# Kernel tuning notes

Measured on AMD Instinct MI355X. Metric: run time of the kernel, lower is better.

Reference implementation:

```python
import jax, jax.numpy as jnp
import numpy as np
import math

NUM_HEADS = 16
SEGMENT_SIZE = 128
DILATION = 2


def hilbert_map(seq_len: int) -> np.ndarray:
    """Boustrophedon ('Hilbert') permutation, matching the torch reference."""
    if seq_len <= 64:
        return np.arange(seq_len, dtype=np.int64)
    g = int(math.ceil(math.sqrt(seq_len)))
    fm = np.zeros(seq_len, dtype=np.int64)
    idx = 0
    for row in range(g):
        cols = range(g) if row % 2 == 0 else range(g - 1, -1, -1)
        for col in cols:
            lp = row * g + col
            if lp < seq_len and idx < seq_len:
                fm[lp] = idx
                idx += 1
    return fm


def setup_inputs() -> dict:
    key = jax.random.key(0)
    k1, k2, k3 = jax.random.split(key, 3)
    B, S, D = 2, 8192, 1024
    x = jax.random.normal(k1, (B, S, D), dtype=jnp.float32)
    W_qkv = jax.random.normal(k2, (D, 3 * D), dtype=jnp.float32) * 0.02
    W_out = jax.random.normal(k3, (D, D), dtype=jnp.float32) * 0.02
    return {"x": x, "W_qkv": W_qkv, "W_out": W_out}


def reference(x, W_qkv, W_out):
    B, S, Dm = x.shape
    H, Dh = NUM_HEADS, Dm // NUM_HEADS
    seg, dil = SEGMENT_SIZE, DILATION
    scale = Dh ** -0.5

    qkv = (x @ W_qkv).reshape(B, S, 3, H, Dh)
    q = jnp.transpose(qkv[:, :, 0], (0, 2, 1, 3))  # [B,H,S,Dh]
    k = jnp.transpose(qkv[:, :, 1], (0, 2, 1, 3))
    v = jnp.transpose(qkv[:, :, 2], (0, 2, 1, 3))

    # Hilbert reorder (active since S > 64)
    m = jnp.asarray(hilbert_map(S))
    q, k, v = q[:, :, m], k[:, :, m], v[:, :, m]

    # Vectorized segment-local dilated attention (S % seg == 0 here)
    nseg = S // seg
    qs = q.reshape(B, H, nseg, seg, Dh)
    ks = k.reshape(B, H, nseg, seg, Dh)[:, :, :, ::dil]  # dilated keys
    vs = v.reshape(B, H, nseg, seg, Dh)[:, :, :, ::dil]
    scores = jnp.einsum('bhnqd,bhnkd->bhnqk', qs, ks) * scale
    attn = jax.nn.softmax(scores, axis=-1)
    out = jnp.einsum('bhnqk,bhnkd->bhnqd', attn, vs).reshape(B, H, S, Dh)

    # Reverse Hilbert ordering
    inv = jnp.argsort(m)
    out = out[:, :, inv]

    out = jnp.transpose(out, (0, 2, 1, 3)).reshape(B, S, Dm)
    return out @ W_out
```

## Files before the change

kernel.cpp:

```cpp
#include <hip/hip_runtime.h>
#include <stdint.h>

typedef unsigned short ushort_t;
typedef __bf16 bf16x8 __attribute__((ext_vector_type(8)));
typedef float  f32x4  __attribute__((ext_vector_type(4)));

#define DEV static __device__ __forceinline__

DEV ushort_t f2bf(float f){
  union { float f; unsigned u; } x; x.f = f;
  unsigned u = x.u;
  return (ushort_t)((u + 0x7fffu + ((u >> 16) & 1u)) >> 16);
}

DEV int hmap(int p){
  int r = p / 91;
  int c = p - r * 91;
  return (r & 1) ? (r * 91 + 90 - c) : p;
}

template<int GATHER>
DEV int arow_map(int r){
  if (GATHER == 0) return r;
  if (GATHER == 1){ int b = r >> 13, p = r & 8191; return b * 8192 + hmap(p); }
  int b = r >> 12, rem = r & 4095, seg = rem >> 6, j = rem & 63;
  return b * 8192 + hmap(seg * 128 + 2 * j);
}

DEV void async16(const void* g, void* l){
  __builtin_amdgcn_global_load_lds(
      (const __attribute__((address_space(1))) unsigned*)g,
      (__attribute__((address_space(3))) unsigned*)l, 16, 0, 0);
}

__global__ void cast_kernel(const float* __restrict__ in, ushort_t* __restrict__ out, int n4){
  int stride = gridDim.x * blockDim.x;
  for (int i = blockIdx.x * blockDim.x + threadIdx.x; i < n4; i += stride){
    float4 v = ((const float4*)in)[i];
    ushort4 o;
    o.x = f2bf(v.x); o.y = f2bf(v.y); o.z = f2bf(v.z); o.w = f2bf(v.w);
    ((ushort4*)out)[i] = o;
  }
}

__global__ void transpose_cast(const float* __restrict__ W, ushort_t* __restrict__ WT,
                               int rows, int cols){
  __shared__ ushort_t t[64 * 66];
  int tid = threadIdx.x;
  int c0 = blockIdx.x * 64, r0 = blockIdx.y * 64;
  int cl = tid & 63, rb = tid >> 6;
  for (int i = 0; i < 16; ++i){
    int r = rb + i * 4;
    t[r * 66 + cl] = f2bf(W[(size_t)(r0 + r) * cols + c0 + cl]);
  }
  __syncthreads();
  int rr = tid & 63, cb = tid >> 6;
  for (int i = 0; i < 16; ++i){
    int cc = cb + i * 4;
    WT[(size_t)(c0 + cc) * rows + r0 + rr] = t[rr * 66 + cc];
  }
}


#define BARRIER() asm volatile("s_barrier" ::: "memory")
#define VMCNT8()  asm volatile("s_waitcnt vmcnt(8)" ::: "memory")
#define VMCNT0()  asm volatile("s_waitcnt vmcnt(0)" ::: "memory")

#define STAGE_A_TO(DST, T1)                                                    \
  {                                                                            \
    _Pragma("unroll") for (int i = 0; i < 4; ++i)                              \
      async16(&A[asrcR[i] + (size_t)(T1) * 64], &DST[i * 4096 + tid * 8]);     \
  }

#define STAGE_B_TO(DST, T1)                                                    \
  {                                                                            \
    _Pragma("unroll") for (int i = 0; i < 4; ++i)                              \
      async16(&BT[bsrcR[i] + (size_t)(T1) * 64], &DST[i * 4096 + tid * 8]);    \
  }

#define COMPUTE(ABUF, BBUF)                                                    \
  {                                                                            \
    bf16x8 bv[4][2];                                                           \
    _Pragma("unroll") for (int ni = 0; ni < 4; ++ni)                           \
      _Pragma("unroll") for (int kk = 0; kk < 2; ++kk)                         \
        bv[ni][kk] = *(const bf16x8*)&BBUF[(wn * 64 + ni * 16 + md) * 64 + axor[kk]]; \
    _Pragma("unroll") for (int kk = 0; kk < 2; ++kk)                           \
      _Pragma("unroll") for (int mi = 0; mi < 8; ++mi){                        \
        bf16x8 af = *(const bf16x8*)&ABUF[(wm * 128 + mi * 16 + md) * 64 + axor[kk]]; \
        _Pragma("unroll") for (int ni = 0; ni < 4; ++ni)                       \
          acc[mi][ni] = __builtin_amdgcn_mfma_f32_16x16x32_bf16(               \
              af, bv[ni][kk], acc[mi][ni], 0, 0, 0);                           \
      }                                                                        \
  }

#define TILE_STEP(CUR, NXT, TSTAGE)                                            \
  {                                                                            \
    if ((TSTAGE) < NT){                                                        \
      STAGE_A_TO(As##NXT, TSTAGE); STAGE_B_TO(Bs##NXT, TSTAGE);                \
      VMCNT8();                                                                \
    } else { VMCNT0(); }                                                       \
    BARRIER();                                                                 \
    COMPUTE(As##CUR, Bs##CUR);                                                 \
    BARRIER();                                                                 \
  }

template<int OUT_BF16, int GATHER>
__global__ __launch_bounds__(512, 2) void gemm_bt(const ushort_t* __restrict__ A,
                                                  const ushort_t* __restrict__ BT,
                                                  void* __restrict__ Cout,
                                                  int M, int N, int K){
  __shared__ __align__(16) ushort_t As0[16384];
  __shared__ __align__(16) ushort_t As1[16384];
  __shared__ __align__(16) ushort_t Bs0[16384];
  __shared__ __align__(16) ushort_t Bs1[16384];
  const int NT = K >> 6;
  int tid = threadIdx.x;
  int lane = tid & 63, w = tid >> 6;
  int md = lane & 15, qd = lane >> 4;
  int wm = w >> 2, wn = w & 3;

  int o = blockIdx.x;
  int mtc = M >> 8;
  int nt = o / mtc, mt = o - nt * mtc;
  int m0 = mt << 8, n0 = nt << 8;

  int rbase = tid >> 3;
  int g0 = ((tid & 7) ^ (rbase & 7)) * 8;
  size_t asrcR[4], bsrcR[4];
  #pragma unroll
  for (int i = 0; i < 4; ++i){
    asrcR[i] = (size_t)arow_map<GATHER>(m0 + i * 64 + rbase) * K + g0;
    bsrcR[i] = (size_t)(n0 + i * 64 + rbase) * K + g0;
  }

  int axor[2] = { (qd ^ (md & 7)) * 8, ((4 + qd) ^ (md & 7)) * 8 };

  f32x4 acc[8][4];
  #pragma unroll
  for (int a = 0; a < 8; ++a)
    #pragma unroll
    for (int b = 0; b < 4; ++b)
      #pragma unroll
      for (int e = 0; e < 4; ++e) acc[a][b][e] = 0.f;

  STAGE_A_TO(As0, 0);
  STAGE_B_TO(Bs0, 0);
  VMCNT0(); BARRIER();

  for (int t = 0; t < NT; t += 2){
    TILE_STEP(0, 1, t + 1);
    TILE_STEP(1, 0, t + 2);
  }

  int crow0 = m0 + wm * 128 + qd * 4;
  int ccol0 = n0 + wn * 64 + md;
  #pragma unroll
  for (int mi = 0; mi < 8; ++mi){
    #pragma unroll
    for (int ni = 0; ni < 4; ++ni){
      f32x4 v = acc[mi][ni];
      #pragma unroll
      for (int r = 0; r < 4; ++r){
        size_t idx = (size_t)(crow0 + mi * 16 + r) * N + ccol0 + ni * 16;
        if (OUT_BF16) ((ushort_t*)Cout)[idx] = f2bf(v[r]);
        else          ((float*)   Cout)[idx] = v[r];
      }
    }
  }
}

__global__ __launch_bounds__(256) void attn_kernel(const ushort_t* __restrict__ Qb,
                                                   const ushort_t* __restrict__ KV,
                                                   ushort_t* __restrict__ aout){
  __shared__ ushort_t Qs[128 * 72];
  __shared__ ushort_t Ks[64 * 72];
  __shared__ ushort_t Vt[64 * 72];
  int tid  = threadIdx.x;
  int lane = tid & 63, w = tid >> 6;
  int qd = lane >> 4, md = lane & 15;
  int seg = blockIdx.x, h = blockIdx.y, b = blockIdx.z;
  int p0 = seg * 128;

  for (int it = 0; it < 4; ++it){
    int q = it * 256 + tid;
    int r = q >> 3, ch = q & 7;
    uint4 d = *(const uint4*)&Qb[(size_t)(b * 8192 + p0 + r) * 1024 + h * 64 + ch * 8];
    *(uint4*)&Qs[r * 72 + ch * 8] = d;
  }
  for (int it = 0; it < 2; ++it){
    int q = it * 256 + tid;
    int r = q >> 3, ch = q & 7;
    uint4 d = *(const uint4*)&KV[(size_t)(b * 4096 + seg * 64 + r) * 2048 + h * 64 + ch * 8];
    *(uint4*)&Ks[r * 72 + ch * 8] = d;
  }
  for (int it = 0; it < 2; ++it){
    int q = it * 256 + tid;
    int r = q >> 3, ch = q & 7;
    union { uint4 v; ushort_t u[8]; } d;
    d.v = *(const uint4*)&KV[(size_t)(b * 4096 + seg * 64 + r) * 2048 + 1024 + h * 64 + ch * 8];
    int kslot = ((r >> 3) ^ ch) * 8 + (r & 7);
    for (int e = 0; e < 8; ++e) Vt[(ch * 8 + e) * 72 + kslot] = d.u[e];
  }
  __syncthreads();

  f32x4 z = {0.f, 0.f, 0.f, 0.f};
  f32x4 sc[2][4];
  for (int mi = 0; mi < 2; ++mi) for (int ni = 0; ni < 4; ++ni) sc[mi][ni] = z;
  for (int kc = 0; kc < 2; ++kc){
    bf16x8 aq[2], bk[4];
    for (int mi = 0; mi < 2; ++mi)
      aq[mi] = *(const bf16x8*)&Qs[(w * 32 + mi * 16 + md) * 72 + kc * 32 + qd * 8];
    for (int ni = 0; ni < 4; ++ni)
      bk[ni] = *(const bf16x8*)&Ks[(ni * 16 + md) * 72 + kc * 32 + qd * 8];
    for (int mi = 0; mi < 2; ++mi)
      for (int ni = 0; ni < 4; ++ni)
        sc[mi][ni] = __builtin_amdgcn_mfma_f32_16x16x32_bf16(aq[mi], bk[ni], sc[mi][ni], 0, 0, 0);
  }

  const float scale = 0.125f;
  ushort_t* Ps = Qs;
  for (int mi = 0; mi < 2; ++mi){
    for (int i = 0; i < 4; ++i){
      float mx = sc[mi][0][i];
      for (int ni = 1; ni < 4; ++ni) mx = fmaxf(mx, sc[mi][ni][i]);
      for (int d = 1; d < 16; d <<= 1) mx = fmaxf(mx, __shfl_xor(mx, d));
      float e[4], sum = 0.f;
      for (int ni = 0; ni < 4; ++ni){ e[ni] = __expf((sc[mi][ni][i] - mx) * scale); sum += e[ni]; }
      for (int d = 1; d < 16; d <<= 1) sum += __shfl_xor(sum, d);
      float inv = 1.0f / sum;
      int r = w * 32 + mi * 16 + qd * 4 + i;
      for (int ni = 0; ni < 4; ++ni)
        Ps[r * 72 + ni * 16 + md] = f2bf(e[ni] * inv);
    }
  }

  f32x4 oc[2][4];
  for (int mi = 0; mi < 2; ++mi) for (int ni = 0; ni < 4; ++ni) oc[mi][ni] = z;
  for (int kc = 0; kc < 2; ++kc){
    bf16x8 ap[2], bv[4];
    for (int mi = 0; mi < 2; ++mi)
      ap[mi] = *(const bf16x8*)&Ps[(w * 32 + mi * 16 + md) * 72 + kc * 32 + qd * 8];
    for (int ni = 0; ni < 4; ++ni){
      int dd = ni * 16 + md;
      int vchunk = ((kc * 4 + qd) ^ ((dd >> 3) & 7)) & 7;
      bv[ni] = *(const bf16x8*)&Vt[dd * 72 + vchunk * 8];
    }
    for (int mi = 0; mi < 2; ++mi)
      for (int ni = 0; ni < 4; ++ni)
        oc[mi][ni] = __builtin_amdgcn_mfma_f32_16x16x32_bf16(ap[mi], bv[ni], oc[mi][ni], 0, 0, 0);
  }

  for (int mi = 0; mi < 2; ++mi){
    for (int i = 0; i < 4; ++i){
      int rl = w * 32 + mi * 16 + qd * 4 + i;
      for (int ni = 0; ni < 4; ++ni)
        Ps[rl * 72 + ni * 16 + md] = f2bf(oc[mi][ni][i]);
    }
  }
  __syncthreads();
  for (int it = 0; it < 4; ++it){
    int q = it * 256 + tid;
    int r = q >> 3, ch = q & 7;
    int s = hmap(p0 + r);
    *(uint4*)&aout[(size_t)(b * 8192 + s) * 1024 + h * 64 + ch * 8] =
        *(const uint4*)&Qs[r * 72 + ch * 8];
  }
}

extern "C" void kernel_launch(void* const* d_in, const int* in_sizes, int n_in,
                              void* d_out, int out_size, void* d_ws, size_t ws_size,
                              hipStream_t stream){
  const float* x    = (const float*)d_in[0];
  const float* Wqkv = (const float*)d_in[1];
  const float* Wout = (const float*)d_in[2];
  float* out = (float*)d_out;

  char* ws = (char*)d_ws;
  ushort_t* xb    = (ushort_t*)(ws);
  ushort_t* WqT   = (ushort_t*)(ws + 33554432);
  ushort_t* WoT   = (ushort_t*)(ws + 39845888);
  ushort_t* Qbuf  = (ushort_t*)(ws + 41943040);
  ushort_t* KVbuf = (ushort_t*)(ws + 75497472);
  ushort_t* aoutb = (ushort_t*)(ws + 109051904);

  cast_kernel<<<2048, 256, 0, stream>>>(x, xb, (16384 * 1024) / 4);
  transpose_cast<<<dim3(48, 16), 256, 0, stream>>>(Wqkv, WqT, 1024, 3072);
  transpose_cast<<<dim3(16, 16), 256, 0, stream>>>(Wout, WoT, 1024, 1024);
  gemm_bt<1, 1><<<dim3(256), dim3(512), 0, stream>>>(xb, WqT, Qbuf, 16384, 1024, 1024);
  gemm_bt<1, 2><<<dim3(256), dim3(512), 0, stream>>>(xb, WqT + (size_t)1024 * 1024, KVbuf, 8192, 2048, 1024);
  attn_kernel<<<dim3(64, 16, 2), 256, 0, stream>>>(Qbuf, KVbuf, aoutb);
  gemm_bt<0, 0><<<dim3(256), dim3(512), 0, stream>>>(aoutb, WoT, out, 16384, 1024, 1024);
}
```

Measured before the change: 266.4 us.

## Switch GEMM to 32x32x16 MFMA and stage bf16 epilogue through LDS

The GEMM inner loop moves from 16x16x32 to 32x32x16 bf16 MFMA tiles. Each wave now holds a 4x2 grid of 16-float accumulators, which cuts LDS fragment reads per MFMA. The bf16 output path writes accumulators into per-wave LDS scratch, reusing the freed A/B buffers with a padded stride of 65. It then reads them back as float4 rows to emit coalesced 4-wide bf16 stores, while the fp32 path keeps scalar stores. The padded-stride float4 LDS reads are not 16-byte aligned, which risks slower or misbehaving LDS accesses, and the larger accumulator layout may change register pressure.

```diff
diff --git a/kernel.cpp b/kernel.cpp
--- a/kernel.cpp
+++ b/kernel.cpp
@@ -4,6 +4,7 @@
 typedef unsigned short ushort_t;
 typedef __bf16 bf16x8 __attribute__((ext_vector_type(8)));
 typedef float  f32x4  __attribute__((ext_vector_type(4)));
+typedef float  f32x16 __attribute__((ext_vector_type(16)));
 
 #define DEV static __device__ __forceinline__
 
@@ -80,15 +81,15 @@
 
 #define COMPUTE(ABUF, BBUF)                                                    \
   {                                                                            \
-    bf16x8 bv[4][2];                                                           \
-    _Pragma("unroll") for (int ni = 0; ni < 4; ++ni)                           \
-      _Pragma("unroll") for (int kk = 0; kk < 2; ++kk)                         \
-        bv[ni][kk] = *(const bf16x8*)&BBUF[(wn * 64 + ni * 16 + md) * 64 + axor[kk]]; \
-    _Pragma("unroll") for (int kk = 0; kk < 2; ++kk)                           \
-      _Pragma("unroll") for (int mi = 0; mi < 8; ++mi){                        \
-        bf16x8 af = *(const bf16x8*)&ABUF[(wm * 128 + mi * 16 + md) * 64 + axor[kk]]; \
-        _Pragma("unroll") for (int ni = 0; ni < 4; ++ni)                       \
-          acc[mi][ni] = __builtin_amdgcn_mfma_f32_16x16x32_bf16(               \
+    bf16x8 bv[2][4];                                                           \
+    _Pragma("unroll") for (int ni = 0; ni < 2; ++ni)                           \
+      _Pragma("unroll") for (int kk = 0; kk < 4; ++kk)                         \
+        bv[ni][kk] = *(const bf16x8*)&BBUF[(wn * 64 + ni * 32 + l31) * 64 + axor[kk]]; \
+    _Pragma("unroll") for (int kk = 0; kk < 4; ++kk)                           \
+      _Pragma("unroll") for (int mi = 0; mi < 4; ++mi){                        \
+        bf16x8 af = *(const bf16x8*)&ABUF[(wm * 128 + mi * 32 + l31) * 64 + axor[kk]]; \
+        _Pragma("unroll") for (int ni = 0; ni < 2; ++ni)                       \
+          acc[mi][ni] = __builtin_amdgcn_mfma_f32_32x32x16_bf16(               \
               af, bv[ni][kk], acc[mi][ni], 0, 0, 0);                           \
       }                                                                        \
   }
@@ -116,7 +117,7 @@
   const int NT = K >> 6;
   int tid = threadIdx.x;
   int lane = tid & 63, w = tid >> 6;
-  int md = lane & 15, qd = lane >> 4;
+  int l31 = lane & 31, lh = lane >> 5;
   int wm = w >> 2, wn = w & 3;
 
   int o = blockIdx.x;
@@ -133,15 +134,18 @@
     bsrcR[i] = (size_t)(n0 + i * 64 + rbase) * K + g0;
   }
 
-  int axor[2] = { (qd ^ (md & 7)) * 8, ((4 + qd) ^ (md & 7)) * 8 };
-
-  f32x4 acc[8][4];
+  int axor[4];
   #pragma unroll
-  for (int a = 0; a < 8; ++a)
+  for (int kk = 0; kk < 4; ++kk)
+    axor[kk] = (((kk << 1) | lh) ^ (l31 & 7)) * 8;
+
+  f32x16 acc[4][2];
+  #pragma unroll
+  for (int a = 0; a < 4; ++a)
     #pragma unroll
-    for (int b = 0; b < 4; ++b)
+    for (int b = 0; b < 2; ++b)
       #pragma unroll
-      for (int e = 0; e < 4; ++e) acc[a][b][e] = 0.f;
+      for (int e = 0; e < 16; ++e) acc[a][b][e] = 0.f;
 
   STAGE_A_TO(As0, 0);
   STAGE_B_TO(Bs0, 0);
@@ -152,20 +156,44 @@
     TILE_STEP(1, 0, t + 2);
   }
 
-  int crow0 = m0 + wm * 128 + qd * 4;
-  int ccol0 = n0 + wn * 64 + md;
-  #pragma unroll
-  for (int mi = 0; mi < 8; ++mi){
+  if (OUT_BF16){
+    float* wbuf;
+    if (w < 3)      wbuf = (float*)As0 + w * 2080;
+    else if (w < 6) wbuf = (float*)As1 + (w - 3) * 2080;
+    else            wbuf = (float*)Bs0 + (w - 6) * 2080;
+    int r16 = lane >> 4, c16 = lane & 15;
     #pragma unroll
-    for (int ni = 0; ni < 4; ++ni){
-      f32x4 v = acc[mi][ni];
+    for (int mi = 0; mi < 4; ++mi){
       #pragma unroll
-      for (int r = 0; r < 4; ++r){
-        size_t idx = (size_t)(crow0 + mi * 16 + r) * N + ccol0 + ni * 16;
-        if (OUT_BF16) ((ushort_t*)Cout)[idx] = f2bf(v[r]);
-        else          ((float*)   Cout)[idx] = v[r];
+      for (int ni = 0; ni < 2; ++ni)
+        #pragma unroll
+        for (int reg = 0; reg < 16; ++reg){
+          int row = (reg & 3) + 8 * (reg >> 2) + 4 * lh;
+          wbuf[row * 65 + ni * 32 + l31] = acc[mi][ni][reg];
+        }
+      #pragma unroll
+      for (int rr = 0; rr < 8; ++rr){
+        int row = rr * 4 + r16;
+        float4 v = *(const float4*)&wbuf[row * 65 + c16 * 4];
+        int grow = m0 + wm * 128 + mi * 32 + row;
+        int gcol = n0 + wn * 64 + c16 * 4;
+        ushort4 ob;
+        ob.x = f2bf(v.x); ob.y = f2bf(v.y); ob.z = f2bf(v.z); ob.w = f2bf(v.w);
+        *(ushort4*)&((ushort_t*)Cout)[(size_t)grow * N + gcol] = ob;
       }
     }
+  } else {
+    #pragma unroll
+    for (int mi = 0; mi < 4; ++mi)
+      #pragma unroll
+      for (int ni = 0; ni < 2; ++ni)
+        #pragma unroll
+        for (int reg = 0; reg < 16; ++reg){
+          int row = (reg & 3) + 8 * (reg >> 2) + 4 * lh;
+          int grow = m0 + wm * 128 + mi * 32 + row;
+          int gcol = n0 + wn * 64 + ni * 32 + l31;
+          ((float*)Cout)[(size_t)grow * N + gcol] = acc[mi][ni][reg];
+        }
   }
 }
 
```

After: 278.5 us. 1.05x slower.

## Merge prep kernels and QKV GEMMs into single launches, stage bf16 epilogue through LDS

Applied to the files above, without the earlier changes.

Combines the x cast and both weight transpose-casts into one prep kernel dispatched by block index. The Q and KV projection GEMMs are merged into one 512-block launch, which cuts kernel count and lets both GEMMs share the GPU at once instead of each filling only 256 blocks. The bf16 output epilogue now stages accumulators through LDS so it can write 8-byte vectorized rows instead of scattered 2-byte stores. The gather mode becomes a runtime argument rather than a template parameter, which adds a little address arithmetic.

```diff
diff --git a/kernel.cpp b/kernel.cpp
--- a/kernel.cpp
+++ b/kernel.cpp
@@ -19,10 +19,9 @@
   return (r & 1) ? (r * 91 + 90 - c) : p;
 }
 
-template<int GATHER>
-DEV int arow_map(int r){
-  if (GATHER == 0) return r;
-  if (GATHER == 1){ int b = r >> 13, p = r & 8191; return b * 8192 + hmap(p); }
+DEV int arow_rt(int r, int gather){
+  if (gather == 0) return r;
+  if (gather == 1){ int b = r >> 13, p = r & 8191; return b * 8192 + hmap(p); }
   int b = r >> 12, rem = r & 4095, seg = rem >> 6, j = rem & 63;
   return b * 8192 + hmap(seg * 128 + 2 * j);
 }
@@ -33,21 +32,29 @@
       (__attribute__((address_space(3))) unsigned*)l, 16, 0, 0);
 }
 
-__global__ void cast_kernel(const float* __restrict__ in, ushort_t* __restrict__ out, int n4){
-  int stride = gridDim.x * blockDim.x;
-  for (int i = blockIdx.x * blockDim.x + threadIdx.x; i < n4; i += stride){
-    float4 v = ((const float4*)in)[i];
-    ushort4 o;
-    o.x = f2bf(v.x); o.y = f2bf(v.y); o.z = f2bf(v.z); o.w = f2bf(v.w);
-    ((ushort4*)out)[i] = o;
-  }
-}
-
-__global__ void transpose_cast(const float* __restrict__ W, ushort_t* __restrict__ WT,
-                               int rows, int cols){
+__global__ __launch_bounds__(256) void prep_kernel(const float* __restrict__ x,
+                                                   const float* __restrict__ Wqkv,
+                                                   const float* __restrict__ Wout,
+                                                   ushort_t* __restrict__ xb,
+                                                   ushort_t* __restrict__ WqT,
+                                                   ushort_t* __restrict__ WoT){
   __shared__ ushort_t t[64 * 66];
-  int tid = threadIdx.x;
-  int c0 = blockIdx.x * 64, r0 = blockIdx.y * 64;
+  int id = blockIdx.x, tid = threadIdx.x;
+  if (id < 2048){
+    const int n4 = (16384 * 1024) / 4;
+    int stride = 2048 * 256;
+    for (int i = id * 256 + tid; i < n4; i += stride){
+      float4 v = ((const float4*)x)[i];
+      ushort4 o;
+      o.x = f2bf(v.x); o.y = f2bf(v.y); o.z = f2bf(v.z); o.w = f2bf(v.w);
+      ((ushort4*)xb)[i] = o;
+    }
+    return;
+  }
+  const float* W; ushort_t* WT; int rows, cols, bx, by;
+  if (id < 2816){ int q = id - 2048; W = Wqkv; WT = WqT; rows = 1024; cols = 3072; bx = q % 48; by = q / 48; }
+  else          { int q = id - 2816; W = Wout; WT = WoT; rows = 1024; cols = 1024; bx = q % 16; by = q / 16; }
+  int c0 = bx * 64, r0 = by * 64;
   int cl = tid & 63, rb = tid >> 6;
   for (int i = 0; i < 16; ++i){
     int r = rb + i * 4;
@@ -104,32 +111,22 @@
     BARRIER();                                                                 \
   }
 
-template<int OUT_BF16, int GATHER>
-__global__ __launch_bounds__(512, 2) void gemm_bt(const ushort_t* __restrict__ A,
-                                                  const ushort_t* __restrict__ BT,
-                                                  void* __restrict__ Cout,
-                                                  int M, int N, int K){
-  __shared__ __align__(16) ushort_t As0[16384];
-  __shared__ __align__(16) ushort_t As1[16384];
-  __shared__ __align__(16) ushort_t Bs0[16384];
-  __shared__ __align__(16) ushort_t Bs1[16384];
+template<int OUT_BF16>
+DEV void gemm_body(const ushort_t* __restrict__ A, const ushort_t* __restrict__ BT,
+                   void* __restrict__ Cout, int N, int K, int gather, int m0, int n0,
+                   ushort_t* As0, ushort_t* As1, ushort_t* Bs0, ushort_t* Bs1){
   const int NT = K >> 6;
   int tid = threadIdx.x;
   int lane = tid & 63, w = tid >> 6;
   int md = lane & 15, qd = lane >> 4;
   int wm = w >> 2, wn = w & 3;
 
-  int o = blockIdx.x;
-  int mtc = M >> 8;
-  int nt = o / mtc, mt = o - nt * mtc;
-  int m0 = mt << 8, n0 = nt << 8;
-
   int rbase = tid >> 3;
   int g0 = ((tid & 7) ^ (rbase & 7)) * 8;
   size_t asrcR[4], bsrcR[4];
   #pragma unroll
   for (int i = 0; i < 4; ++i){
-    asrcR[i] = (size_t)arow_map<GATHER>(m0 + i * 64 + rbase) * K + g0;
+    asrcR[i] = (size_t)arow_rt(m0 + i * 64 + rbase, gather) * K + g0;
     bsrcR[i] = (size_t)(n0 + i * 64 + rbase) * K + g0;
   }
 
@@ -152,21 +149,75 @@
     TILE_STEP(1, 0, t + 2);
   }
 
-  int crow0 = m0 + wm * 128 + qd * 4;
-  int ccol0 = n0 + wn * 64 + md;
-  #pragma unroll
-  for (int mi = 0; mi < 8; ++mi){
+  if (OUT_BF16){
+    float* wbuf = (w < 4) ? ((float*)As0 + w * 1040) : ((float*)As1 + (w - 4) * 1040);
+    int r16 = lane >> 4, c16 = lane & 15;
     #pragma unroll
-    for (int ni = 0; ni < 4; ++ni){
-      f32x4 v = acc[mi][ni];
+    for (int mi = 0; mi < 8; ++mi){
       #pragma unroll
-      for (int r = 0; r < 4; ++r){
-        size_t idx = (size_t)(crow0 + mi * 16 + r) * N + ccol0 + ni * 16;
-        if (OUT_BF16) ((ushort_t*)Cout)[idx] = f2bf(v[r]);
-        else          ((float*)   Cout)[idx] = v[r];
+      for (int ni = 0; ni < 4; ++ni)
+        #pragma unroll
+        for (int reg = 0; reg < 4; ++reg)
+          wbuf[(qd * 4 + reg) * 65 + ni * 16 + md] = acc[mi][ni][reg];
+      #pragma unroll
+      for (int rr = 0; rr < 4; ++rr){
+        int row = rr * 4 + r16;
+        float4 v = *(const float4*)&wbuf[row * 65 + c16 * 4];
+        int grow = m0 + wm * 128 + mi * 16 + row;
+        int gcol = n0 + wn * 64 + c16 * 4;
+        ushort4 ob;
+        ob.x = f2bf(v.x); ob.y = f2bf(v.y); ob.z = f2bf(v.z); ob.w = f2bf(v.w);
+        *(ushort4*)&((ushort_t*)Cout)[(size_t)grow * N + gcol] = ob;
       }
     }
-  }
+  } else {
+    #pragma unroll
+    for (int mi = 0; mi < 8; ++mi)
+      #pragma unroll
+      for (int ni = 0; ni < 4; ++ni){
+        f32x4 v = acc[mi][ni];
+        #pragma unroll
+        for (int reg = 0; reg < 4; ++reg){
+          int grow = m0 + wm * 128 + mi * 16 + qd * 4 + reg;
+          int gcol = n0 + wn * 64 + ni * 16 + md;
+          ((float*)Cout)[(size_t)grow * N + gcol] = v[reg];
+        }
+      }
+  }
+}
+
+__global__ __launch_bounds__(512, 2) void gemm_qkv(const ushort_t* __restrict__ xb,
+                                                   const ushort_t* __restrict__ WqT,
+                                                   ushort_t* __restrict__ Qbuf,
+                                                   ushort_t* __restrict__ KVbuf){
+  __shared__ __align__(16) ushort_t As0[16384];
+  __shared__ __align__(16) ushort_t As1[16384];
+  __shared__ __align__(16) ushort_t Bs0[16384];
+  __shared__ __align__(16) ushort_t Bs1[16384];
+  int id = blockIdx.x;
+  const ushort_t* BT; ushort_t* C; int N, gather, m0, n0;
+  if (id < 256){
+    int o = id;
+    m0 = (o & 63) << 8; n0 = (o >> 6) << 8;
+    BT = WqT; C = Qbuf; N = 1024; gather = 1;
+  } else {
+    int o = id - 256;
+    m0 = (o & 31) << 8; n0 = (o >> 5) << 8;
+    BT = WqT + (size_t)1024 * 1024; C = KVbuf; N = 2048; gather = 2;
+  }
+  gemm_body<1>(xb, BT, C, N, 1024, gather, m0, n0, As0, As1, Bs0, Bs1);
+}
+
+__global__ __launch_bounds__(512, 2) void gemm_out(const ushort_t* __restrict__ aoutb,
+                                                   const ushort_t* __restrict__ WoT,
+                                                   float* __restrict__ out){
+  __shared__ __align__(16) ushort_t As0[16384];
+  __shared__ __align__(16) ushort_t As1[16384];
+  __shared__ __align__(16) ushort_t Bs0[16384];
+  __shared__ __align__(16) ushort_t Bs1[16384];
+  int o = blockIdx.x;
+  int m0 = (o & 63) << 8, n0 = (o >> 6) << 8;
+  gemm_body<0>(aoutb, WoT, out, 1024, 1024, 0, m0, n0, As0, As1, Bs0, Bs1);
 }
 
 __global__ __launch_bounds__(256) void attn_kernel(const ushort_t* __restrict__ Qb,
@@ -283,11 +334,8 @@
   ushort_t* KVbuf = (ushort_t*)(ws + 75497472);
   ushort_t* aoutb = (ushort_t*)(ws + 109051904);
 
-  cast_kernel<<<2048, 256, 0, stream>>>(x, xb, (16384 * 1024) / 4);
-  transpose_cast<<<dim3(48, 16), 256, 0, stream>>>(Wqkv, WqT, 1024, 3072);
-  transpose_cast<<<dim3(16, 16), 256, 0, stream>>>(Wout, WoT, 1024, 1024);
-  gemm_bt<1, 1><<<dim3(256), dim3(512), 0, stream>>>(xb, WqT, Qbuf, 16384, 1024, 1024);
-  gemm_bt<1, 2><<<dim3(256), dim3(512), 0, stream>>>(xb, WqT + (size_t)1024 * 1024, KVbuf, 8192, 2048, 1024);
+  prep_kernel<<<3072, 256, 0, stream>>>(x, Wqkv, Wout, xb, WqT, WoT);
+  gemm_qkv<<<512, 512, 0, stream>>>(xb, WqT, Qbuf, KVbuf);
   attn_kernel<<<dim3(64, 16, 2), 256, 0, stream>>>(Qbuf, KVbuf, aoutb);
-  gemm_bt<0, 0><<<dim3(256), dim3(512), 0, stream>>>(aoutb, WoT, out, 16384, 1024, 1024);
-}
+  gemm_out<<<256, 512, 0, stream>>>(aoutb, WoT, out);
+}
```

Measured after the change: 267.3 us. About the same (+0.3%).
